# Performance work log

Hardware: AMD Instinct MI355X
Metric: run time of the kernel (lower is better)

## Reference

```python
import jax, jax.numpy as jnp
import numpy as np

H = 768
NH = 12
HD = H // NH
FF = 3072
EPS = 1e-12
SCALE = 1.0 / (HD ** 0.5)


def _ln(x, g, b):
    m = jnp.mean(x, axis=-1, keepdims=True)
    v = jnp.mean((x - m) ** 2, axis=-1, keepdims=True)
    return (x - m) * jax.lax.rsqrt(v + EPS) * g + b


def setup_inputs() -> dict:
    key = jax.random.key(0)
    ks = jax.random.split(key, 16)
    B, Q, S, T = 8, 64, 48, 128
    s = 0.02
    return {
        "q": jax.random.normal(ks[0], (B, Q, H), jnp.float32),
        "k": jax.random.normal(ks[1], (B, S, T, H), jnp.float32),
        "mask": jax.random.randint(ks[2], (B, S, T), 0, 2, jnp.int32),
        "Wq": jax.random.normal(ks[3], (H, H), jnp.float32) * s,
        "Wkv": jax.random.normal(ks[4], (H, H), jnp.float32) * s,
        "Wo": jax.random.normal(ks[5], (H, H), jnp.float32) * s,
        "bo": jnp.zeros((H,), jnp.float32),
        "ln1_g": jnp.ones((H,), jnp.float32),
        "ln1_b": jnp.zeros((H,), jnp.float32),
        "W1": jax.random.normal(ks[6], (H, FF), jnp.float32) * s,
        "b1": jnp.zeros((FF,), jnp.float32),
        "W2": jax.random.normal(ks[7], (FF, H), jnp.float32) * s,
        "b2": jnp.zeros((H,), jnp.float32),
        "ln2_g": jnp.ones((H,), jnp.float32),
        "ln2_b": jnp.zeros((H,), jnp.float32),
    }


def reference(q, k, mask, Wq, Wkv, Wo, bo, ln1_g, ln1_b, W1, b1, W2, b2, ln2_g, ln2_b):
    B, Q, _ = q.shape
    _, S, T, _ = k.shape
    # projections (no bias)
    qp = (q @ Wq).reshape(B, Q, NH, HD)            # [b,q,h,d]
    kv = (k @ Wkv).reshape(B, S, T, NH, HD)        # [b,s,t,h,d]
    # broadcast-query grouped attention: softmax only over token dim t
    scores = jnp.einsum('bqhd,bsthd->bhqst', qp, kv) * SCALE
    scores = scores + mask.astype(scores.dtype)[:, None, None, :, :] * -10000.0
    alpha = jax.nn.softmax(scores, axis=-1)        # dropout is identity in eval
    res = jnp.einsum('bhqst,bsthd->bqshd', alpha, kv).reshape(B, Q, S, H)
    # BertSelfOutput with zero residual (residual=False)
    attn_out = _ln(res @ Wo + bo, ln1_g, ln1_b)    # [b,q,s,H]
    # FFN
    ffn = jax.nn.gelu(attn_out @ W1 + b1, approximate=False) @ W2 + b2
    return _ln(attn_out + ffn, ln2_g, ln2_b)
```

## Files before the change

kernel.cpp:

```cpp
#include <hip/hip_runtime.h>
#include <hip/hip_bf16.h>
#include <math.h>

#define B_ 8
#define Q_ 64
#define S_ 48
#define T_ 128
#define H_ 768
#define NH_ 12
#define HD_ 64
#define FF_ 3072

typedef float f32x4 __attribute__((ext_vector_type(4)));
typedef short s16x8 __attribute__((ext_vector_type(8)));
typedef short s16x4 __attribute__((ext_vector_type(4)));

__device__ __forceinline__ float ldT(const float* p, size_t i) { return p[i]; }
__device__ __forceinline__ float ldT(const __hip_bfloat16* p, size_t i) { return __bfloat162float(p[i]); }
__device__ __forceinline__ void stT(float* p, size_t i, float v) { p[i] = v; }
__device__ __forceinline__ void stT(__hip_bfloat16* p, size_t i, float v) { p[i] = __float2bfloat16(v); }

__device__ __forceinline__ short f2bf(float f) {
  __hip_bfloat16 h = __float2bfloat16(f);
  return *reinterpret_cast<short*>(&h);
}

__device__ __forceinline__ float gelu_f(float x) {
  return 0.5f * x * (1.0f + erff(x * 0.70710678118654752f));
}

__device__ __forceinline__ void gld_lds16(const void* g, void* l) {
  __builtin_amdgcn_global_load_lds(
      (const __attribute__((address_space(1))) void*)g,
      (__attribute__((address_space(3))) void*)l, 16, 0, 0);
}

__device__ __forceinline__ int swz_off(int row, int kc) {
  return row * 64 + ((kc ^ ((row >> 1) & 3)) << 4);
}

template<typename OT, bool BIAS, bool GELU>
__global__ __launch_bounds__(256) void gemm_mfma(
    const __hip_bfloat16* __restrict__ A,
    const __hip_bfloat16* __restrict__ BT,
    const float* __restrict__ bias, OT* __restrict__ C,
    int N, int K, int nbx)
{
  __shared__ char sm[2][16384];

  int wg = blockIdx.x;
  const int q8 = gridDim.x >> 3;
  wg = (wg & 7) * q8 + (wg >> 3);
  const int bm = wg / nbx;
  const int bn = wg % nbx;
  const int m0 = bm * 128, n0 = bn * 128;

  const int tid = threadIdx.x;
  const int lane = tid & 63;
  const int wid = tid >> 6;
  const int wr = wid >> 1, wc = wid & 1;

  const int nt = K >> 5;

  auto stage = [&](int buf, int kt) {
    const int k0 = kt << 5;
    const __hip_bfloat16* Ab = A + (size_t)m0 * K + k0;
    const __hip_bfloat16* Bb = BT + (size_t)n0 * K + k0;
    char* smA = sm[buf];
    char* smB = sm[buf] + 8192;
    #pragma unroll
    for (int r = 0; r < 2; ++r) {
      const int c = tid + r * 256;
      const int row = c >> 2, slot = c & 3;
      const int kc = slot ^ ((row >> 1) & 3);
      gld_lds16(Ab + (size_t)row * K + kc * 8, smA + c * 16);
      gld_lds16(Bb + (size_t)row * K + kc * 8, smB + c * 16);
    }
  };

  f32x4 acc[4][4] = {};
  stage(0, 0);

  for (int kt = 0; kt < nt; ++kt) {
    __syncthreads();
    if (kt + 1 < nt) stage((kt + 1) & 1, kt + 1);
    const char* smA = sm[kt & 1];
    const char* smB = sm[kt & 1] + 8192;
    const int kc = lane >> 4, rl = lane & 15;
    s16x8 af[4], bf[4];
    #pragma unroll
    for (int m = 0; m < 4; ++m)
      af[m] = *(const s16x8*)(smA + swz_off(wr * 64 + m * 16 + rl, kc));
    #pragma unroll
    for (int n = 0; n < 4; ++n)
      bf[n] = *(const s16x8*)(smB + swz_off(wc * 64 + n * 16 + rl, kc));
    #pragma unroll
    for (int m = 0; m < 4; ++m)
      #pragma unroll
      for (int n = 0; n < 4; ++n)
        acc[m][n] = __builtin_amdgcn_mfma_f32_16x16x32_bf16(af[m], bf[n], acc[m][n], 0, 0, 0);
  }

  const int colb = n0 + wc * 64 + (lane & 15);
  const int rowb = m0 + wr * 64 + (lane >> 4) * 4;
  #pragma unroll
  for (int n = 0; n < 4; ++n) {
    const int col = colb + n * 16;
    const float bv = BIAS ? bias[col] : 0.0f;
    #pragma unroll
    for (int m = 0; m < 4; ++m) {
      #pragma unroll
      for (int r = 0; r < 4; ++r) {
        const int row = rowb + m * 16 + r;
        float v = acc[m][n][r] + bv;
        if (GELU) v = gelu_f(v);
        stT(C, (size_t)row * N + col, v);
      }
    }
  }
}

template<typename OT>
__global__ __launch_bounds__(256) void gemm64(
    const float* __restrict__ A, const float* __restrict__ W,
    OT* __restrict__ C, int M, int N, int K)
{
  __shared__ float As[16][65];
  __shared__ float Ws[16][65];
  const int tid = threadIdx.x;
  const int m0 = blockIdx.y * 64;
  const int n0 = blockIdx.x * 64;
  const int tx = (tid & 15) * 4;
  const int ty = (tid >> 4) * 4;
  float acc[4][4] = {};

  for (int k0 = 0; k0 < K; k0 += 16) {
    #pragma unroll
    for (int r = 0; r < 4; ++r) {
      int idx = tid + r * 256;
      int mm = idx >> 4, kk = idx & 15;
      As[kk][mm] = A[(size_t)(m0 + mm) * K + (k0 + kk)];
    }
    #pragma unroll
    for (int r = 0; r < 4; ++r) {
      int idx = tid + r * 256;
      int kk = idx >> 6, nn = idx & 63;
      Ws[kk][nn] = W[(size_t)(k0 + kk) * N + (n0 + nn)];
    }
    __syncthreads();
    #pragma unroll
    for (int kk = 0; kk < 16; ++kk) {
      float a[4], b[4];
      #pragma unroll
      for (int i = 0; i < 4; ++i) a[i] = As[kk][ty + i];
      #pragma unroll
      for (int j = 0; j < 4; ++j) b[j] = Ws[kk][tx + j];
      #pragma unroll
      for (int i = 0; i < 4; ++i)
        #pragma unroll
        for (int j = 0; j < 4; ++j) acc[i][j] += a[i] * b[j];
    }
    __syncthreads();
  }
  #pragma unroll
  for (int i = 0; i < 4; ++i)
    #pragma unroll
    for (int j = 0; j < 4; ++j)
      stT(C, (size_t)(m0 + ty + i) * N + (n0 + tx + j), acc[i][j]);
}

__global__ __launch_bounds__(256) void transpose_cast(
    const float* __restrict__ W, __hip_bfloat16* __restrict__ WT, int K, int N)
{
  __shared__ float t[32][33];
  const int n0 = blockIdx.x * 32, k0 = blockIdx.y * 32;
  const int x = threadIdx.x & 31, y4 = (threadIdx.x >> 5) * 4;
  #pragma unroll
  for (int i = 0; i < 4; ++i)
    t[y4 + i][x] = W[(size_t)(k0 + y4 + i) * N + n0 + x];
  __syncthreads();
  #pragma unroll
  for (int i = 0; i < 4; ++i)
    WT[(size_t)(n0 + y4 + i) * K + k0 + x] = __float2bfloat16(t[x][y4 + i]);
}

__global__ __launch_bounds__(256) void cast_f32_bf16(
    const float* __restrict__ x, __hip_bfloat16* __restrict__ y, size_t n4)
{
  const size_t i = (size_t)blockIdx.x * 256 + threadIdx.x;
  if (i >= n4) return;
  const float4 v = ((const float4*)x)[i];
  __hip_bfloat16 o[4] = { __float2bfloat16(v.x), __float2bfloat16(v.y),
                          __float2bfloat16(v.z), __float2bfloat16(v.w) };
  *(ushort4*)(y + i * 4) = *(ushort4*)o;
}

__global__ __launch_bounds__(256) void attn_mfma(
    const __hip_bfloat16* __restrict__ qp,
    const __hip_bfloat16* __restrict__ kvp,
    const int* __restrict__ mask,
    __hip_bfloat16* __restrict__ res)
{
  const int s = blockIdx.x, h = blockIdx.y, b = blockIdx.z;
  __shared__ __align__(16) char lds[66048];
  char* Ks = lds;
  char* VT = lds + 16384;
  char* SC = lds + 32768;
  float* mv = (float*)(lds + 65536);

  const int tid = threadIdx.x;
  const int lane = tid & 63;
  const int wid = tid >> 6;
  const int wr = wid >> 1, wc = wid & 1;
  const int kcg = lane >> 4, rl = lane & 15;

  if (tid < 128) mv[tid] = (float)mask[((size_t)b * S_ + s) * T_ + tid] * -10000.0f;

  {
    const __hip_bfloat16* qb = qp + ((size_t)b * Q_) * H_ + h * HD_;
    #pragma unroll
    for (int r = 0; r < 2; ++r) {
      const int c = tid + r * 256;
      const int qq = c >> 3, sc = c & 7;
      const int kc8 = sc ^ (qq & 7);
      gld_lds16(qb + (size_t)qq * H_ + kc8 * 8, SC + c * 16);
    }
  }
  {
    const int kc8 = tid & 7, tg = tid >> 3;
    const int t0 = tg * 4;
    const __hip_bfloat16* kb = kvp + (((size_t)b * S_ + s) * T_) * H_ + h * HD_ + kc8 * 8;
    s16x8 r0 = *(const s16x8*)(kb + (size_t)(t0 + 0) * H_);
    s16x8 r1 = *(const s16x8*)(kb + (size_t)(t0 + 1) * H_);
    s16x8 r2 = *(const s16x8*)(kb + (size_t)(t0 + 2) * H_);
    s16x8 r3 = *(const s16x8*)(kb + (size_t)(t0 + 3) * H_);
    *(s16x8*)(Ks + (t0 + 0) * 128 + ((kc8 ^ ((t0 + 0) & 7)) << 4)) = r0;
    *(s16x8*)(Ks + (t0 + 1) * 128 + ((kc8 ^ ((t0 + 1) & 7)) << 4)) = r1;
    *(s16x8*)(Ks + (t0 + 2) * 128 + ((kc8 ^ ((t0 + 2) & 7)) << 4)) = r2;
    *(s16x8*)(Ks + (t0 + 3) * 128 + ((kc8 ^ ((t0 + 3) & 7)) << 4)) = r3;
    const int tc = tg >> 1;
    const int toff = (tg & 1) * 8;
    #pragma unroll
    for (int j = 0; j < 8; ++j) {
      s16x4 v4 = { r0[j], r1[j], r2[j], r3[j] };
      const int d = kc8 * 8 + j;
      *(s16x4*)(VT + d * 256 + ((tc ^ (d & 15)) << 4) + toff) = v4;
    }
  }
  __syncthreads();

  f32x4 acc[2][4] = {};
  {
    s16x8 af[2][2], bf[2][4];
    #pragma unroll
    for (int kk = 0; kk < 2; ++kk) {
      #pragma unroll
      for (int m = 0; m < 2; ++m) {
        const int q = wr * 32 + m * 16 + rl;
        const int kc8 = kk * 4 + kcg;
        af[kk][m] = *(const s16x8*)(SC + q * 128 + ((kc8 ^ (q & 7)) << 4));
      }
      #pragma unroll
      for (int n = 0; n < 4; ++n) {
        const int t = wc * 64 + n * 16 + rl;
        const int kc8 = kk * 4 + kcg;
        bf[kk][n] = *(const s16x8*)(Ks + t * 128 + ((kc8 ^ (t & 7)) << 4));
      }
    }
    #pragma unroll
    for (int kk = 0; kk < 2; ++kk)
      #pragma unroll
      for (int m = 0; m < 2; ++m)
        #pragma unroll
        for (int n = 0; n < 4; ++n)
          acc[m][n] = __builtin_amdgcn_mfma_f32_16x16x32_bf16(af[kk][m], bf[kk][n], acc[m][n], 0, 0, 0);
  }
  __syncthreads();

  #pragma unroll
  for (int m = 0; m < 2; ++m)
    #pragma unroll
    for (int n = 0; n < 4; ++n)
      #pragma unroll
      for (int r = 0; r < 4; ++r) {
        const int q = wr * 32 + m * 16 + (lane >> 4) * 4 + r;
        const int t = wc * 64 + n * 16 + rl;
        const int tc32 = t >> 2;
        *(float*)(SC + q * 512 + ((tc32 ^ (q & 31)) << 4) + (t & 3) * 4) =
            acc[m][n][r] * 0.125f + mv[t];
      }
  __syncthreads();

  {
    const int q = tid >> 2, quarter = tid & 3;
    float vals[32];
    #pragma unroll
    for (int j = 0; j < 8; ++j) {
      const int tc32 = quarter * 8 + j;
      const f32x4 c = *(const f32x4*)(SC + q * 512 + ((tc32 ^ (q & 31)) << 4));
      vals[j * 4 + 0] = c[0]; vals[j * 4 + 1] = c[1];
      vals[j * 4 + 2] = c[2]; vals[j * 4 + 3] = c[3];
    }
    float mx = -1e30f;
    #pragma unroll
    for (int i = 0; i < 32; ++i) mx = fmaxf(mx, vals[i]);
    mx = fmaxf(mx, __shfl_xor(mx, 1, 64));
    mx = fmaxf(mx, __shfl_xor(mx, 2, 64));
    float sum = 0.0f;
    #pragma unroll
    for (int i = 0; i < 32; ++i) { vals[i] = expf(vals[i] - mx); sum += vals[i]; }
    sum += __shfl_xor(sum, 1, 64);
    sum += __shfl_xor(sum, 2, 64);
    const float inv = 1.0f / sum;
    #pragma unroll
    for (int jj = 0; jj < 4; ++jj) {
      const int tcp = quarter * 4 + jj;
      s16x8 pk;
      #pragma unroll
      for (int i = 0; i < 8; ++i) pk[i] = f2bf(vals[jj * 8 + i] * inv);
      *(s16x8*)(SC + q * 512 + ((tcp ^ (q & 15)) << 4)) = pk;
    }
  }
  __syncthreads();

  f32x4 oacc[2][2] = {};
  #pragma unroll
  for (int kt = 0; kt < 4; ++kt) {
    s16x8 pa[2], vb[2];
    #pragma unroll
    for (int m = 0; m < 2; ++m) {
      const int q = wr * 32 + m * 16 + rl;
      const int tcp = kt * 4 + kcg;
      pa[m] = *(const s16x8*)(SC + q * 512 + ((tcp ^ (q & 15)) << 4));
    }
    #pragma unroll
    for (int n = 0; n < 2; ++n) {
      const int d = wc * 32 + n * 16 + rl;
      const int tc = kt * 4 + kcg;
      vb[n] = *(const s16x8*)(VT + d * 256 + ((tc ^ (d & 15)) << 4));
    }
    #pragma unroll
    for (int m = 0; m < 2; ++m)
      #pragma unroll
      for (int n = 0; n < 2; ++n)
        oacc[m][n] = __builtin_amdgcn_mfma_f32_16x16x32_bf16(pa[m], vb[n], oacc[m][n], 0, 0, 0);
  }
  #pragma unroll
  for (int m = 0; m < 2; ++m)
    #pragma unroll
    for (int n = 0; n < 2; ++n)
      #pragma unroll
      for (int r = 0; r < 4; ++r) {
        const int q = wr * 32 + m * 16 + (lane >> 4) * 4 + r;
        const int d = wc * 32 + n * 16 + rl;
        res[(((size_t)b * Q_ + q) * S_ + s) * H_ + h * HD_ + d] =
            __float2bfloat16(oacc[m][n][r]);
      }
}

template<bool ADD, typename IT, typename OT>
__global__ __launch_bounds__(256) void ln_kernel(
    const IT* __restrict__ X, const IT* __restrict__ X2,
    const float* __restrict__ g, const float* __restrict__ bta,
    OT* __restrict__ Y)
{
  const size_t row = blockIdx.x;
  const int tid = threadIdx.x;
  float v[3];
  #pragma unroll
  for (int i = 0; i < 3; ++i) {
    int c = tid + i * 256;
    v[i] = ldT(X, row * H_ + c);
    if (ADD) v[i] += ldT(X2, row * H_ + c);
  }
  float sum = v[0] + v[1] + v[2];
  #pragma unroll
  for (int off = 32; off > 0; off >>= 1) sum += __shfl_down(sum, off, 64);
  __shared__ float red[8];
  const int w = tid >> 6;
  if ((tid & 63) == 0) red[w] = sum;
  __syncthreads();
  const float mean = (red[0] + red[1] + red[2] + red[3]) * (1.0f / 768.0f);
  float vs = 0.0f;
  #pragma unroll
  for (int i = 0; i < 3; ++i) { v[i] -= mean; vs += v[i] * v[i]; }
  #pragma unroll
  for (int off = 32; off > 0; off >>= 1) vs += __shfl_down(vs, off, 64);
  if ((tid & 63) == 0) red[4 + w] = vs;
  __syncthreads();
  const float rstd = rsqrtf((red[4] + red[5] + red[6] + red[7]) * (1.0f / 768.0f) + 1e-12f);
  #pragma unroll
  for (int i = 0; i < 3; ++i) {
    int c = tid + i * 256;
    stT(Y, row * H_ + c, v[i] * rstd * g[c] + bta[c]);
  }
}

extern "C" void kernel_launch(void* const* d_in, const int* in_sizes, int n_in,
                              void* d_out, int out_size, void* d_ws, size_t ws_size,
                              hipStream_t stream) {
  const float* q    = (const float*)d_in[0];
  const float* k    = (const float*)d_in[1];
  const int*   mask = (const int*)d_in[2];
  const float* Wq   = (const float*)d_in[3];
  const float* Wkv  = (const float*)d_in[4];
  const float* Wo   = (const float*)d_in[5];
  const float* bo   = (const float*)d_in[6];
  const float* ln1g = (const float*)d_in[7];
  const float* ln1b = (const float*)d_in[8];
  const float* W1   = (const float*)d_in[9];
  const float* b1   = (const float*)d_in[10];
  const float* W2   = (const float*)d_in[11];
  const float* b2   = (const float*)d_in[12];
  const float* ln2g = (const float*)d_in[13];
  const float* ln2b = (const float*)d_in[14];
  float* out = (float*)d_out;

  const int MROWS = B_ * Q_ * S_;
  const int KVROWS = B_ * S_ * T_;

  char* ws = (char*)d_ws;
  __hip_bfloat16* kbf  = (__hip_bfloat16*)ws;
  __hip_bfloat16* kvp  = (__hip_bfloat16*)(ws + 75497472);
  __hip_bfloat16* ffn1 = (__hip_bfloat16*)ws;
  __hip_bfloat16* ares = (__hip_bfloat16*)(ws + 150994944);
  __hip_bfloat16* ffn2 = ares;
  __hip_bfloat16* aln  = (__hip_bfloat16*)(ws + 188743680);
  __hip_bfloat16* qp   = (__hip_bfloat16*)(ws + 226492416);
  __hip_bfloat16* WkvT = (__hip_bfloat16*)(ws + 228065280);
  __hip_bfloat16* WoT  = (__hip_bfloat16*)(ws + 229244928);
  __hip_bfloat16* W1T  = (__hip_bfloat16*)(ws + 230424576);
  __hip_bfloat16* W2T  = (__hip_bfloat16*)(ws + 235143168);

  dim3 blk(256);

  transpose_cast<<<dim3(24, 24), blk, 0, stream>>>(Wkv, WkvT, H_, H_);
  transpose_cast<<<dim3(24, 24), blk, 0, stream>>>(Wo, WoT, H_, H_);
  transpose_cast<<<dim3(96, 24), blk, 0, stream>>>(W1, W1T, H_, FF_);
  transpose_cast<<<dim3(24, 96), blk, 0, stream>>>(W2, W2T, FF_, H_);
  cast_f32_bf16<<<dim3((KVROWS * H_ / 4 + 255) / 256), blk, 0, stream>>>(
      k, kbf, (size_t)KVROWS * H_ / 4);

  gemm64<__hip_bfloat16><<<dim3(H_ / 64, 512 / 64), blk, 0, stream>>>(
      q, Wq, qp, 512, H_, H_);
  gemm_mfma<__hip_bfloat16, false, false>
      <<<dim3((KVROWS / 128) * (H_ / 128)), blk, 0, stream>>>(
      kbf, WkvT, nullptr, kvp, H_, H_, H_ / 128);
  attn_mfma<<<dim3(S_, NH_, B_), blk, 0, stream>>>(qp, kvp, mask, ares);
  gemm_mfma<float, true, false>
      <<<dim3((MROWS / 128) * (H_ / 128)), blk, 0, stream>>>(
      ares, WoT, bo, out, H_, H_, H_ / 128);
  ln_kernel<false, float, __hip_bfloat16><<<MROWS, blk, 0, stream>>>(
      out, nullptr, ln1g, ln1b, aln);
  gemm_mfma<__hip_bfloat16, true, true>
      <<<dim3((MROWS / 128) * (FF_ / 128)), blk, 0, stream>>>(
      aln, W1T, b1, ffn1, FF_, H_, FF_ / 128);
  gemm_mfma<__hip_bfloat16, true, false>
      <<<dim3((MROWS / 128) * (H_ / 128)), blk, 0, stream>>>(
      ffn1, W2T, b2, ffn2, H_, FF_, H_ / 128);
  ln_kernel<true, __hip_bfloat16, float><<<MROWS, blk, 0, stream>>>(
      aln, ffn2, ln2g, ln2b, out);
}
```

Before: 684.2 us.

## Replace bf16 GEMM with 8-wave, triple-buffered, 128x256-tile pipelined MFMA kernel

Replaces the 256-thread double-buffered 128x128 GEMM with a 512-thread kernel that computes 128x256 output tiles with K-step 64. It uses three LDS buffers, splits global-to-LDS staging into thirds, and interleaves those loads with MFMA quarter-blocks using explicit barriers, vmcnt waits and setprio. The goal is to hide global load latency and improve operand reuse for the four large GEMMs. In exchange it uses 144KB of LDS per block, which limits occupancy, and it requires K/64 to be divisible by 3.

```diff
diff --git a/kernel.cpp b/kernel.cpp
--- a/kernel.cpp
+++ b/kernel.cpp
@@ -35,86 +35,195 @@
       (__attribute__((address_space(3))) void*)l, 16, 0, 0);
 }
 
-__device__ __forceinline__ int swz_off(int row, int kc) {
-  return row * 64 + ((kc ^ ((row >> 1) & 3)) << 4);
-}
-
-template<typename OT, bool BIAS, bool GELU>
-__global__ __launch_bounds__(256) void gemm_mfma(
+#define FENCE() asm volatile("" ::: "memory")
+#define BARRIER() do { FENCE(); __builtin_amdgcn_s_barrier(); FENCE(); } while (0)
+#define WAITV(n) asm volatile("s_waitcnt vmcnt(" #n ")" ::: "memory")
+
+template<int K, typename OT, bool BIAS, bool GELU>
+__global__ __launch_bounds__(512, 2) void gemm8p(
     const __hip_bfloat16* __restrict__ A,
     const __hip_bfloat16* __restrict__ BT,
     const float* __restrict__ bias, OT* __restrict__ C,
-    int N, int K, int nbx)
+    int N, int nbx)
 {
-  __shared__ char sm[2][16384];
+  constexpr int NT = K / 64;
+  static_assert(NT % 3 == 0, "K/64 must be divisible by 3");
+  __shared__ __align__(16) char sm[3 * 49152];
 
   int wg = blockIdx.x;
   const int q8 = gridDim.x >> 3;
   wg = (wg & 7) * q8 + (wg >> 3);
   const int bm = wg / nbx;
   const int bn = wg % nbx;
-  const int m0 = bm * 128, n0 = bn * 128;
+  const int m0 = bm * 128, n0 = bn * 256;
 
   const int tid = threadIdx.x;
   const int lane = tid & 63;
   const int wid = tid >> 6;
-  const int wr = wid >> 1, wc = wid & 1;
-
-  const int nt = K >> 5;
-
-  auto stage = [&](int buf, int kt) {
-    const int k0 = kt << 5;
-    const __hip_bfloat16* Ab = A + (size_t)m0 * K + k0;
-    const __hip_bfloat16* Bb = BT + (size_t)n0 * K + k0;
-    char* smA = sm[buf];
-    char* smB = sm[buf] + 8192;
-    #pragma unroll
-    for (int r = 0; r < 2; ++r) {
-      const int c = tid + r * 256;
-      const int row = c >> 2, slot = c & 3;
-      const int kc = slot ^ ((row >> 1) & 3);
-      gld_lds16(Ab + (size_t)row * K + kc * 8, smA + c * 16);
-      gld_lds16(Bb + (size_t)row * K + kc * 8, smB + c * 16);
-    }
+  const int wr = wid >> 2;
+  const int wc = wid & 3;
+  const int kcg = lane >> 4;
+  const int rl = lane & 15;
+
+  const __hip_bfloat16* gA[2];
+  const __hip_bfloat16* gB[4];
+  #pragma unroll
+  for (int r = 0; r < 2; ++r) {
+    const int c = tid + r * 512, row = c >> 3, slot = c & 7;
+    const int kc = slot ^ (row & 7);
+    gA[r] = A + (size_t)(m0 + row) * K + kc * 8;
+  }
+  #pragma unroll
+  for (int r = 0; r < 4; ++r) {
+    const int c = tid + r * 512, row = c >> 3, slot = c & 7;
+    const int kc = slot ^ (row & 7);
+    gB[r] = BT + (size_t)(n0 + row) * K + kc * 8;
+  }
+
+  auto stageA = [&](char* bb) {
+    gld_lds16(gA[0], bb + tid * 16);
+    gld_lds16(gA[1], bb + (tid + 512) * 16);
+    gA[0] += 64; gA[1] += 64;
   };
+  auto stageB1 = [&](char* bb) {
+    gld_lds16(gB[0], bb + 16384 + tid * 16);
+    gld_lds16(gB[1], bb + 16384 + (tid + 512) * 16);
+    gB[0] += 64; gB[1] += 64;
+  };
+  auto stageB2 = [&](char* bb) {
+    gld_lds16(gB[2], bb + 16384 + (tid + 1024) * 16);
+    gld_lds16(gB[3], bb + 16384 + (tid + 1536) * 16);
+    gB[2] += 64; gB[3] += 64;
+  };
+
+  int offA[4][2], offB[4][2];
+  #pragma unroll
+  for (int mf = 0; mf < 4; ++mf)
+    #pragma unroll
+    for (int kch = 0; kch < 2; ++kch) {
+      const int row = wr * 64 + mf * 16 + rl;
+      const int ch = kch * 4 + kcg;
+      offA[mf][kch] = row * 128 + ((ch ^ (row & 7)) << 4);
+    }
+  #pragma unroll
+  for (int nf = 0; nf < 4; ++nf)
+    #pragma unroll
+    for (int kch = 0; kch < 2; ++kch) {
+      const int row = wc * 64 + nf * 16 + rl;
+      const int ch = kch * 4 + kcg;
+      offB[nf][kch] = 16384 + row * 128 + ((ch ^ (row & 7)) << 4);
+    }
 
   f32x4 acc[4][4] = {};
-  stage(0, 0);
-
-  for (int kt = 0; kt < nt; ++kt) {
-    __syncthreads();
-    if (kt + 1 < nt) stage((kt + 1) & 1, kt + 1);
-    const char* smA = sm[kt & 1];
-    const char* smB = sm[kt & 1] + 8192;
-    const int kc = lane >> 4, rl = lane & 15;
-    s16x8 af[4], bf[4];
-    #pragma unroll
-    for (int m = 0; m < 4; ++m)
-      af[m] = *(const s16x8*)(smA + swz_off(wr * 64 + m * 16 + rl, kc));
-    #pragma unroll
-    for (int n = 0; n < 4; ++n)
-      bf[n] = *(const s16x8*)(smB + swz_off(wc * 64 + n * 16 + rl, kc));
-    #pragma unroll
-    for (int m = 0; m < 4; ++m)
-      #pragma unroll
-      for (int n = 0; n < 4; ++n)
-        acc[m][n] = __builtin_amdgcn_mfma_f32_16x16x32_bf16(af[m], bf[n], acc[m][n], 0, 0, 0);
-  }
-
-  const int colb = n0 + wc * 64 + (lane & 15);
+
+  stageA(sm); stageB1(sm); stageB2(sm);
+  stageA(sm + 49152); stageB1(sm + 49152); stageB2(sm + 49152);
+  WAITV(6);
+  BARRIER();
+
+  auto tile_body = [&](char* cb, char* nb, bool doStage, bool last) {
+    s16x8 af[4][2], bf[4][2];
+    #pragma unroll
+    for (int mf = 0; mf < 2; ++mf)
+      #pragma unroll
+      for (int kch = 0; kch < 2; ++kch)
+        af[mf][kch] = *(const s16x8*)(cb + offA[mf][kch]);
+    #pragma unroll
+    for (int nf = 0; nf < 2; ++nf)
+      #pragma unroll
+      for (int kch = 0; kch < 2; ++kch)
+        bf[nf][kch] = *(const s16x8*)(cb + offB[nf][kch]);
+    if (doStage) stageA(nb);
+    BARRIER();
+    __builtin_amdgcn_s_setprio(1);
+    #pragma unroll
+    for (int kch = 0; kch < 2; ++kch)
+      #pragma unroll
+      for (int mf = 0; mf < 2; ++mf)
+        #pragma unroll
+        for (int nf = 0; nf < 2; ++nf)
+          acc[mf][nf] = __builtin_amdgcn_mfma_f32_16x16x32_bf16(
+              af[mf][kch], bf[nf][kch], acc[mf][nf], 0, 0, 0);
+    __builtin_amdgcn_s_setprio(0);
+    BARRIER();
+    #pragma unroll
+    for (int nf = 2; nf < 4; ++nf)
+      #pragma unroll
+      for (int kch = 0; kch < 2; ++kch)
+        bf[nf][kch] = *(const s16x8*)(cb + offB[nf][kch]);
+    if (doStage) stageB1(nb);
+    BARRIER();
+    __builtin_amdgcn_s_setprio(1);
+    #pragma unroll
+    for (int kch = 0; kch < 2; ++kch)
+      #pragma unroll
+      for (int mf = 0; mf < 2; ++mf)
+        #pragma unroll
+        for (int nf = 2; nf < 4; ++nf)
+          acc[mf][nf] = __builtin_amdgcn_mfma_f32_16x16x32_bf16(
+              af[mf][kch], bf[nf][kch], acc[mf][nf], 0, 0, 0);
+    __builtin_amdgcn_s_setprio(0);
+    BARRIER();
+    #pragma unroll
+    for (int mf = 2; mf < 4; ++mf)
+      #pragma unroll
+      for (int kch = 0; kch < 2; ++kch)
+        af[mf][kch] = *(const s16x8*)(cb + offA[mf][kch]);
+    if (doStage) stageB2(nb);
+    BARRIER();
+    __builtin_amdgcn_s_setprio(1);
+    #pragma unroll
+    for (int kch = 0; kch < 2; ++kch)
+      #pragma unroll
+      for (int mf = 2; mf < 4; ++mf)
+        #pragma unroll
+        for (int nf = 0; nf < 2; ++nf)
+          acc[mf][nf] = __builtin_amdgcn_mfma_f32_16x16x32_bf16(
+              af[mf][kch], bf[nf][kch], acc[mf][nf], 0, 0, 0);
+    __builtin_amdgcn_s_setprio(0);
+    BARRIER();
+    __builtin_amdgcn_s_setprio(1);
+    #pragma unroll
+    for (int kch = 0; kch < 2; ++kch)
+      #pragma unroll
+      for (int mf = 2; mf < 4; ++mf)
+        #pragma unroll
+        for (int nf = 2; nf < 4; ++nf)
+          acc[mf][nf] = __builtin_amdgcn_mfma_f32_16x16x32_bf16(
+              af[mf][kch], bf[nf][kch], acc[mf][nf], 0, 0, 0);
+    __builtin_amdgcn_s_setprio(0);
+    if (!last) {
+      if (doStage) WAITV(6);
+      else         WAITV(0);
+      BARRIER();
+    }
+  };
+
+  char* b0 = sm;
+  char* b1 = sm + 49152;
+  char* b2 = sm + 2 * 49152;
+  #pragma unroll 1
+  for (int t = 0; t < NT; t += 3) {
+    tile_body(b0, b2, t + 2 < NT, t + 1 == NT);
+    tile_body(b1, b0, t + 3 < NT, t + 2 == NT);
+    tile_body(b2, b1, t + 4 < NT, t + 3 == NT);
+  }
+
+  const int colb = n0 + wc * 64 + rl;
   const int rowb = m0 + wr * 64 + (lane >> 4) * 4;
-  #pragma unroll
-  for (int n = 0; n < 4; ++n) {
-    const int col = colb + n * 16;
-    const float bv = BIAS ? bias[col] : 0.0f;
-    #pragma unroll
-    for (int m = 0; m < 4; ++m) {
-      #pragma unroll
-      for (int r = 0; r < 4; ++r) {
-        const int row = rowb + m * 16 + r;
-        float v = acc[m][n][r] + bv;
+  float bv[4];
+  #pragma unroll
+  for (int nf = 0; nf < 4; ++nf) bv[nf] = BIAS ? bias[colb + nf * 16] : 0.0f;
+  #pragma unroll
+  for (int mf = 0; mf < 4; ++mf) {
+    #pragma unroll
+    for (int r = 0; r < 4; ++r) {
+      const int row = rowb + mf * 16 + r;
+      #pragma unroll
+      for (int nf = 0; nf < 4; ++nf) {
+        float v = acc[mf][nf][r] + bv[nf];
         if (GELU) v = gelu_f(v);
-        stT(C, (size_t)row * N + col, v);
+        stT(C, (size_t)row * N + colb + nf * 16, v);
       }
     }
   }
@@ -433,6 +542,7 @@
   __hip_bfloat16* W2T  = (__hip_bfloat16*)(ws + 235143168);
 
   dim3 blk(256);
+  dim3 blk8(512);
 
   transpose_cast<<<dim3(24, 24), blk, 0, stream>>>(Wkv, WkvT, H_, H_);
   transpose_cast<<<dim3(24, 24), blk, 0, stream>>>(Wo, WoT, H_, H_);
@@ -443,21 +553,21 @@
 
   gemm64<__hip_bfloat16><<<dim3(H_ / 64, 512 / 64), blk, 0, stream>>>(
       q, Wq, qp, 512, H_, H_);
-  gemm_mfma<__hip_bfloat16, false, false>
-      <<<dim3((KVROWS / 128) * (H_ / 128)), blk, 0, stream>>>(
-      kbf, WkvT, nullptr, kvp, H_, H_, H_ / 128);
+  gemm8p<768, __hip_bfloat16, false, false>
+      <<<dim3((KVROWS / 128) * (H_ / 256)), blk8, 0, stream>>>(
+      kbf, WkvT, nullptr, kvp, H_, H_ / 256);
   attn_mfma<<<dim3(S_, NH_, B_), blk, 0, stream>>>(qp, kvp, mask, ares);
-  gemm_mfma<float, true, false>
-      <<<dim3((MROWS / 128) * (H_ / 128)), blk, 0, stream>>>(
-      ares, WoT, bo, out, H_, H_, H_ / 128);
+  gemm8p<768, float, true, false>
+      <<<dim3((MROWS / 128) * (H_ / 256)), blk8, 0, stream>>>(
+      ares, WoT, bo, out, H_, H_ / 256);
   ln_kernel<false, float, __hip_bfloat16><<<MROWS, blk, 0, stream>>>(
       out, nullptr, ln1g, ln1b, aln);
-  gemm_mfma<__hip_bfloat16, true, true>
-      <<<dim3((MROWS / 128) * (FF_ / 128)), blk, 0, stream>>>(
-      aln, W1T, b1, ffn1, FF_, H_, FF_ / 128);
-  gemm_mfma<__hip_bfloat16, true, false>
-      <<<dim3((MROWS / 128) * (H_ / 128)), blk, 0, stream>>>(
-      ffn1, W2T, b2, ffn2, H_, FF_, H_ / 128);
+  gemm8p<768, __hip_bfloat16, true, true>
+      <<<dim3((MROWS / 128) * (FF_ / 256)), blk8, 0, stream>>>(
+      aln, W1T, b1, ffn1, FF_, FF_ / 256);
+  gemm8p<3072, __hip_bfloat16, true, false>
+      <<<dim3((MROWS / 128) * (H_ / 256)), blk8, 0, stream>>>(
+      ffn1, W2T, b2, ffn2, H_, H_ / 256);
   ln_kernel<true, __hip_bfloat16, float><<<MROWS, blk, 0, stream>>>(
       aln, ffn2, ln2g, ln2b, out);
 }
```

New measurement: 679.7 us. Within noise of the previous version (-0.7%).
